# Kernel tuning notes

Measured on AMD Instinct MI355X. Metric: run time of the kernel, lower is better.

## Reference

```python
import jax, jax.numpy as jnp
import numpy as np

D = 512   # in_dim
W = 8     # window
B = 8192  # batch


def _l2norm(x):
    # matches torch.nn.functional.normalize(p=2, dim=-1, eps=1e-12)
    n = jnp.linalg.norm(x, axis=-1, keepdims=True)
    return x / jnp.maximum(n, 1e-12)


def setup_inputs() -> dict:
    key = jax.random.key(0)
    ks = jax.random.split(key, 15)
    s = 1.0 / np.sqrt(D)  # torch nn.Linear default init range
    u = lambda k, shape: jax.random.uniform(k, shape, jnp.float32, -s, s)
    return {
        "x": jax.random.normal(ks[0], (B, (2 * W + 1) * D), jnp.float32),
        "Wq": u(ks[1], (D, D)), "bq": u(ks[2], (D,)),
        "Wkc": u(ks[3], (D, D)), "bkc": u(ks[4], (D,)),
        "Wkp": u(ks[5], (W, D, D)), "bkp": u(ks[6], (W, D)),
        "Wkn": u(ks[7], (W, D, D)), "bkn": u(ks[8], (W, D)),
        "Wfp": u(ks[9], (W, D, D)), "bfp": u(ks[10], (W, D)),
        "Wfn": u(ks[11], (W, D, D)), "bfn": u(ks[12], (W, D)),
        "Wfc": u(ks[13], (D, D)), "bfc": u(ks[14], (D,)),
    }


def reference(x, Wq, bq, Wkc, bkc, Wkp, bkp, Wkn, bkn, Wfp, bfp, Wfn, bfn, Wfc, bfc):
    b = x.shape[0]
    xp = x[:, : W * D].reshape(b, W, D)             # prev chunks [B,W,D]
    xc = x[:, W * D : (W + 1) * D]                  # center      [B,D]
    xn = x[:, (W + 1) * D :].reshape(b, W, D)       # next chunks [B,W,D]

    q = xc @ Wq.T + bq                              # [B,D]
    kc = xc @ Wkc.T + bkc
    attn_c = jnp.sum(q * kc, axis=-1, keepdims=True)  # [B,1]

    # per-offset key projections, batched over the W offsets
    kp = jnp.einsum('bwd,wed->bwe', xp, Wkp) + bkp  # [B,W,D]
    kn = jnp.einsum('bwd,wed->bwe', xn, Wkn) + bkn
    ap = jnp.einsum('bd,bwd->bw', q, kp)            # [B,W]
    an = jnp.einsum('bd,bwd->bw', q, kn)

    xc_ = (xc * attn_c
           + jnp.einsum('bw,bwd->bd', ap, xp)
           + jnp.einsum('bw,bwd->bd', an, xn))

    # per-offset feed-forward + l2 normalize (dropout = identity at eval)
    xp_out = _l2norm(jnp.einsum('bwd,wed->bwe', xp, Wfp) + bfp)
    xn_out = _l2norm(jnp.einsum('bwd,wed->bwe', xn, Wfn) + bfn)

    xc_ = _l2norm(xc_)
    xc_ = xc_ @ Wfc.T + bfc
    xc_ = _l2norm(xc_ + xc)

    return jnp.concatenate([xp_out.reshape(b, W * D), xc_, xn_out.reshape(b, W * D)], axis=1)
```

## Files before the change

kernel.cpp:

```cpp
#include <hip/hip_runtime.h>
#include <stdint.h>

#define D 512
#define NW 8
#define BATCH 8192
#define XROW 8704
#define BM 128
#define BK 64
#define MAT 262144

typedef __attribute__((ext_vector_type(8))) short bf16x8;
typedef __attribute__((ext_vector_type(4))) float f32x4;

struct Params {
  const float* x;
  const float* bq; const float* bkc;
  const float* bkp; const float* bkn;
  const float* bfp; const float* bfn;
  const float* bfc;
  const unsigned short* Wb;
  unsigned short* qw;
  unsigned short* kcw;
  float* ap; float* an;
  float* xcn;
  float* out;
};

__device__ __forceinline__ unsigned short f2bf(float f) {
  union { float f; unsigned u; } v; v.f = f;
  unsigned u = v.u + 0x7FFFu + ((v.u >> 16) & 1u);
  return (unsigned short)(u >> 16);
}
__device__ __forceinline__ float bf2f(unsigned short h) {
  union { unsigned u; float f; } v; v.u = ((unsigned)h) << 16;
  return v.f;
}

__global__ void convert_weights(const float* Wq, const float* Wkc, const float* Wkp,
                                const float* Wkn, const float* Wfp, const float* Wfn,
                                const float* Wfc, unsigned short* outw) {
  const int total4 = 35 * MAT / 4;
  for (int i4 = blockIdx.x * blockDim.x + threadIdx.x; i4 < total4;
       i4 += gridDim.x * blockDim.x) {
    int idx = i4 * 4;
    int m = idx >> 18;
    int e = idx & (MAT - 1);
    const float* src;
    if (m == 0)       src = Wq + e;
    else if (m == 1)  src = Wkc + e;
    else if (m < 10)  src = Wkp + (size_t)(m - 2) * MAT + e;
    else if (m < 18)  src = Wkn + (size_t)(m - 10) * MAT + e;
    else if (m < 26)  src = Wfp + (size_t)(m - 18) * MAT + e;
    else if (m < 34)  src = Wfn + (size_t)(m - 26) * MAT + e;
    else              src = Wfc + e;
    float4 v = *reinterpret_cast<const float4*>(src);
    ushort4 o;
    o.x = f2bf(v.x); o.y = f2bf(v.y); o.z = f2bf(v.z); o.w = f2bf(v.w);
    *reinterpret_cast<ushort4*>(outw + idx) = o;
  }
}

__launch_bounds__(512)
__global__ void gemm_mega(Params p, int launch_id) {
  __shared__ unsigned short Alds[BM * BK];
  __shared__ unsigned short Blds[D * BK];

  const int nchunk = gridDim.x >> 3;
  const int swz  = (blockIdx.x & 7) * nchunk + (blockIdx.x >> 3);
  const int unit = swz >> 6;
  const int mb   = swz & 63;
  const int t    = threadIdx.x;
  const int lane = t & 63;
  const int wave = t >> 6;
  const int wm   = wave >> 2;
  const int wn   = wave & 3;

  const float* Aptr = p.x;
  int lda = XROW;
  int aofs = 0;
  const unsigned short* Wm = p.Wb;
  const float* bias = p.bq;
  int epi = 0;
  int outofs = 0;
  float* dotdst = nullptr;
  int wofs = 0;

  if (launch_id == 0) {
    if (unit == 0)      { aofs = 8 * D; Wm = p.Wb;            bias = p.bq;  epi = 0; }
    else if (unit == 1) { aofs = 8 * D; Wm = p.Wb + MAT;      bias = p.bkc; epi = 1; }
    else if (unit < 10) { int w = unit - 2;  aofs = w * D;
                          Wm = p.Wb + (size_t)(18 + w) * MAT; bias = p.bfp + w * D;
                          epi = 2; outofs = w * D; }
    else                { int w = unit - 10; aofs = (9 + w) * D;
                          Wm = p.Wb + (size_t)(26 + w) * MAT; bias = p.bfn + w * D;
                          epi = 2; outofs = (9 + w) * D; }
  } else if (launch_id == 1) {
    if (unit < 8) { int w = unit;     aofs = w * D;
                    Wm = p.Wb + (size_t)(2 + w) * MAT;  bias = p.bkp + w * D;
                    epi = 3; dotdst = p.ap; wofs = w; }
    else          { int w = unit - 8; aofs = (9 + w) * D;
                    Wm = p.Wb + (size_t)(10 + w) * MAT; bias = p.bkn + w * D;
                    epi = 3; dotdst = p.an; wofs = w; }
  } else {
    Aptr = p.xcn; lda = D; aofs = 0;
    Wm = p.Wb + (size_t)34 * MAT; bias = p.bfc; epi = 4; outofs = 8 * D;
  }

  const int row0 = mb * BM;

  f32x4 acc[4][8];
#pragma unroll
  for (int m = 0; m < 4; ++m)
#pragma unroll
    for (int n = 0; n < 8; ++n)
      acc[m][n] = (f32x4){0.f, 0.f, 0.f, 0.f};

  const int ar = t >> 2;
  const int ak = (t & 3) * 16;
  const float* a_src = Aptr + (size_t)(row0 + ar) * lda + aofs + ak;

  char* albase = (char*)Alds;
  char* blbase = (char*)Blds;

  for (int kt = 0; kt < 8; ++kt) {
    const int k0 = kt * BK;
    float4 av0 = *reinterpret_cast<const float4*>(a_src + k0);
    float4 av1 = *reinterpret_cast<const float4*>(a_src + k0 + 4);
    float4 av2 = *reinterpret_cast<const float4*>(a_src + k0 + 8);
    float4 av3 = *reinterpret_cast<const float4*>(a_src + k0 + 12);
    {
      bf16x8 pk;
      pk[0] = (short)f2bf(av0.x); pk[1] = (short)f2bf(av0.y);
      pk[2] = (short)f2bf(av0.z); pk[3] = (short)f2bf(av0.w);
      pk[4] = (short)f2bf(av1.x); pk[5] = (short)f2bf(av1.y);
      pk[6] = (short)f2bf(av1.z); pk[7] = (short)f2bf(av1.w);
      int bo = (ar << 7) + (ak << 1);
      *reinterpret_cast<bf16x8*>(albase + (bo ^ ((bo >> 3) & 0x70))) = pk;
      pk[0] = (short)f2bf(av2.x); pk[1] = (short)f2bf(av2.y);
      pk[2] = (short)f2bf(av2.z); pk[3] = (short)f2bf(av2.w);
      pk[4] = (short)f2bf(av3.x); pk[5] = (short)f2bf(av3.y);
      pk[6] = (short)f2bf(av3.z); pk[7] = (short)f2bf(av3.w);
      bo += 16;
      *reinterpret_cast<bf16x8*>(albase + (bo ^ ((bo >> 3) & 0x70))) = pk;
    }
#pragma unroll
    for (int i = 0; i < 8; ++i) {
      int o = i * 8192 + wave * 1024 + lane * 16;
      int Ls = o ^ ((o >> 3) & 0x70);
      const unsigned short* src = Wm + (size_t)(Ls >> 7) * D + k0 + ((Ls & 127) >> 1);
      __builtin_amdgcn_global_load_lds(
          (const __attribute__((address_space(1))) unsigned*)src,
          (__attribute__((address_space(3))) unsigned*)(blbase + i * 8192 + wave * 1024),
          16, 0, 0);
    }
    __syncthreads();
#pragma unroll
    for (int ks = 0; ks < 2; ++ks) {
      const int kb = ks * 64 + ((lane >> 4) << 4);
      bf16x8 af[4], bfr[8];
#pragma unroll
      for (int m = 0; m < 4; ++m) {
        int r = wm * 64 + m * 16 + (lane & 15);
        int bo = (r << 7) + kb;
        af[m] = *reinterpret_cast<const bf16x8*>(albase + (bo ^ ((bo >> 3) & 0x70)));
      }
#pragma unroll
      for (int n = 0; n < 8; ++n) {
        int r = wn * 128 + n * 16 + (lane & 15);
        int bo = (r << 7) + kb;
        bfr[n] = *reinterpret_cast<const bf16x8*>(blbase + (bo ^ ((bo >> 3) & 0x70)));
      }
#pragma unroll
      for (int m = 0; m < 4; ++m)
#pragma unroll
        for (int n = 0; n < 8; ++n)
          acc[m][n] = __builtin_amdgcn_mfma_f32_16x16x32_bf16(af[m], bfr[n], acc[m][n], 0, 0, 0);
    }
    __syncthreads();
  }

  float* red = (float*)Alds;
  const int rj = (lane >> 4) * 4;
  const int cl = lane & 15;
  float bv[8];
#pragma unroll
  for (int n = 0; n < 8; ++n) bv[n] = bias[wn * 128 + n * 16 + cl];
#pragma unroll
  for (int m = 0; m < 4; ++m)
#pragma unroll
    for (int n = 0; n < 8; ++n)
#pragma unroll
      for (int j = 0; j < 4; ++j)
        acc[m][n][j] += bv[n];

  if (epi <= 1) {
    unsigned short* dst = (epi == 0) ? p.qw : p.kcw;
#pragma unroll
    for (int m = 0; m < 4; ++m)
#pragma unroll
      for (int j = 0; j < 4; ++j) {
        int r = wm * 64 + m * 16 + rj + j;
#pragma unroll
        for (int n = 0; n < 8; ++n) {
          int col = wn * 128 + n * 16 + cl;
          dst[(size_t)(row0 + r) * D + col] = f2bf(acc[m][n][j]);
        }
      }
  } else if (epi == 3) {
    if (t < BM) red[t] = 0.f;
    __syncthreads();
#pragma unroll
    for (int m = 0; m < 4; ++m)
#pragma unroll
      for (int j = 0; j < 4; ++j) {
        int r = wm * 64 + m * 16 + rj + j;
        float s = 0.f;
#pragma unroll
        for (int n = 0; n < 8; ++n) {
          int col = wn * 128 + n * 16 + cl;
          s += acc[m][n][j] * bf2f(p.qw[(size_t)(row0 + r) * D + col]);
        }
        s += __shfl_xor(s, 1); s += __shfl_xor(s, 2);
        s += __shfl_xor(s, 4); s += __shfl_xor(s, 8);
        if (cl == 0) atomicAdd(&red[r], s);
      }
    __syncthreads();
    if (t < BM) dotdst[(size_t)(row0 + t) * NW + wofs] = red[t];
  } else {
    if (epi == 4) {
#pragma unroll
      for (int m = 0; m < 4; ++m)
#pragma unroll
        for (int j = 0; j < 4; ++j) {
          int r = wm * 64 + m * 16 + rj + j;
#pragma unroll
          for (int n = 0; n < 8; ++n) {
            int col = wn * 128 + n * 16 + cl;
            acc[m][n][j] += p.x[(size_t)(row0 + r) * XROW + 8 * D + col];
          }
        }
    }
    if (t < BM) red[t] = 0.f;
    __syncthreads();
#pragma unroll
    for (int m = 0; m < 4; ++m)
#pragma unroll
      for (int j = 0; j < 4; ++j) {
        int r = wm * 64 + m * 16 + rj + j;
        float s = 0.f;
#pragma unroll
        for (int n = 0; n < 8; ++n) s += acc[m][n][j] * acc[m][n][j];
        s += __shfl_xor(s, 1); s += __shfl_xor(s, 2);
        s += __shfl_xor(s, 4); s += __shfl_xor(s, 8);
        if (cl == 0) atomicAdd(&red[r], s);
      }
    __syncthreads();
#pragma unroll
    for (int m = 0; m < 4; ++m)
#pragma unroll
      for (int j = 0; j < 4; ++j) {
        int r = wm * 64 + m * 16 + rj + j;
        float sc = 1.f / fmaxf(sqrtf(red[r]), 1e-12f);
#pragma unroll
        for (int n = 0; n < 8; ++n) {
          int col = wn * 128 + n * 16 + cl;
          p.out[(size_t)(row0 + r) * XROW + outofs + col] = acc[m][n][j] * sc;
        }
      }
  }
}

__launch_bounds__(128)
__global__ void combine(Params p) {
  __shared__ float sbuf[2];
  __shared__ float swt[16];
  const int b = blockIdx.x;
  const int t = threadIdx.x;
  const float* xrow = p.x + (size_t)b * XROW;

  const ushort4 q4 = reinterpret_cast<const ushort4*>(p.qw + (size_t)b * D)[t];
  const ushort4 c4 = reinterpret_cast<const ushort4*>(p.kcw + (size_t)b * D)[t];
  float s = bf2f(q4.x) * bf2f(c4.x) + bf2f(q4.y) * bf2f(c4.y) +
            bf2f(q4.z) * bf2f(c4.z) + bf2f(q4.w) * bf2f(c4.w);
  for (int m = 32; m >= 1; m >>= 1) s += __shfl_xor(s, m);
  if ((t & 63) == 0) sbuf[t >> 6] = s;
  if (t < 8)       swt[t] = p.ap[(size_t)b * NW + t];
  else if (t < 16) swt[t] = p.an[(size_t)b * NW + (t - 8)];
  __syncthreads();
  const float att = sbuf[0] + sbuf[1];

  float4 xc4 = reinterpret_cast<const float4*>(xrow + 8 * D)[t];
  float4 v;
  v.x = xc4.x * att; v.y = xc4.y * att; v.z = xc4.z * att; v.w = xc4.w * att;
#pragma unroll
  for (int w = 0; w < 8; ++w) {
    float aw = swt[w], nw2 = swt[8 + w];
    float4 xp4 = reinterpret_cast<const float4*>(xrow + w * D)[t];
    float4 xn4 = reinterpret_cast<const float4*>(xrow + (9 + w) * D)[t];
    v.x += aw * xp4.x + nw2 * xn4.x;
    v.y += aw * xp4.y + nw2 * xn4.y;
    v.z += aw * xp4.z + nw2 * xn4.z;
    v.w += aw * xp4.w + nw2 * xn4.w;
  }
  float ss = v.x * v.x + v.y * v.y + v.z * v.z + v.w * v.w;
  __syncthreads();
  for (int m = 32; m >= 1; m >>= 1) ss += __shfl_xor(ss, m);
  if ((t & 63) == 0) sbuf[t >> 6] = ss;
  __syncthreads();
  float sc = 1.f / fmaxf(sqrtf(sbuf[0] + sbuf[1]), 1e-12f);
  float4 o; o.x = v.x * sc; o.y = v.y * sc; o.z = v.z * sc; o.w = v.w * sc;
  reinterpret_cast<float4*>(p.xcn + (size_t)b * D)[t] = o;
}

extern "C" void kernel_launch(void* const* d_in, const int* in_sizes, int n_in,
                              void* d_out, int out_size, void* d_ws, size_t ws_size,
                              hipStream_t stream) {
  const float* x   = (const float*)d_in[0];
  const float* Wq  = (const float*)d_in[1];
  const float* bq  = (const float*)d_in[2];
  const float* Wkc = (const float*)d_in[3];
  const float* bkc = (const float*)d_in[4];
  const float* Wkp = (const float*)d_in[5];
  const float* bkp = (const float*)d_in[6];
  const float* Wkn = (const float*)d_in[7];
  const float* bkn = (const float*)d_in[8];
  const float* Wfp = (const float*)d_in[9];
  const float* bfp = (const float*)d_in[10];
  const float* Wfn = (const float*)d_in[11];
  const float* bfn = (const float*)d_in[12];
  const float* Wfc = (const float*)d_in[13];
  const float* bfc = (const float*)d_in[14];

  char* ws = (char*)d_ws;
  unsigned short* Wb  = (unsigned short*)ws;
  unsigned short* qw  = (unsigned short*)(ws + 18350080);
  unsigned short* kcw = (unsigned short*)(ws + 26738688);
  float* ap  = (float*)(ws + 35127296);
  float* an  = (float*)(ws + 35389440);
  float* xcn = (float*)(ws + 35651584);

  Params p { x, bq, bkc, bkp, bkn, bfp, bfn, bfc, Wb, qw, kcw, ap, an, xcn, (float*)d_out };

  hipLaunchKernelGGL(convert_weights, dim3(2048), dim3(256), 0, stream,
                     Wq, Wkc, Wkp, Wkn, Wfp, Wfn, Wfc, Wb);
  hipLaunchKernelGGL(gemm_mega, dim3(18 * 64), dim3(512), 0, stream, p, 0);
  hipLaunchKernelGGL(gemm_mega, dim3(16 * 64), dim3(512), 0, stream, p, 1);
  hipLaunchKernelGGL(combine,   dim3(8192),   dim3(128), 0, stream, p);
  hipLaunchKernelGGL(gemm_mega, dim3(64),     dim3(512), 0, stream, p, 2);
}
```

Baseline: 870.4 us.

## Pre-convert x to bf16 and double-buffer GEMM loads with async global-to-LDS

Adds a bf16 copy of the whole input x to the conversion kernel, so the GEMM can load A tiles with direct global-to-LDS loads, the same way it loads weights. The GEMM main loop becomes a two-stage double-buffered pipeline with BK=32 and 16 k-steps, using explicit vmcnt waits, barriers and raised priority around the MFMA block. The combine kernel now writes its normalized output as bf16 for the final GEMM. The aim is to overlap memory traffic with compute and drop in-loop fp32 conversion, at the cost of an extra full pass over x (read fp32, write bf16) and a larger workspace.

```diff
diff --git a/kernel.cpp b/kernel.cpp
--- a/kernel.cpp
+++ b/kernel.cpp
@@ -6,7 +6,8 @@
 #define BATCH 8192
 #define XROW 8704
 #define BM 128
-#define BK 64
+#define BK 32
+#define KT 16
 #define MAT 262144
 
 typedef __attribute__((ext_vector_type(8))) short bf16x8;
@@ -19,10 +20,11 @@
   const float* bfp; const float* bfn;
   const float* bfc;
   const unsigned short* Wb;
+  const unsigned short* xb;
   unsigned short* qw;
   unsigned short* kcw;
   float* ap; float* an;
-  float* xcn;
+  unsigned short* xcn;
   float* out;
 };
 
@@ -36,34 +38,47 @@
   return v.f;
 }
 
-__global__ void convert_weights(const float* Wq, const float* Wkc, const float* Wkp,
-                                const float* Wkn, const float* Wfp, const float* Wfn,
-                                const float* Wfc, unsigned short* outw) {
-  const int total4 = 35 * MAT / 4;
+__global__ void convert_all(const float* x, const float* Wq, const float* Wkc,
+                            const float* Wkp, const float* Wkn, const float* Wfp,
+                            const float* Wfn, const float* Wfc,
+                            unsigned short* Wb, unsigned short* xb) {
+  const int totW = 35 * MAT;
+  const int total4 = (totW + BATCH * XROW) / 4;
   for (int i4 = blockIdx.x * blockDim.x + threadIdx.x; i4 < total4;
        i4 += gridDim.x * blockDim.x) {
     int idx = i4 * 4;
-    int m = idx >> 18;
-    int e = idx & (MAT - 1);
     const float* src;
-    if (m == 0)       src = Wq + e;
-    else if (m == 1)  src = Wkc + e;
-    else if (m < 10)  src = Wkp + (size_t)(m - 2) * MAT + e;
-    else if (m < 18)  src = Wkn + (size_t)(m - 10) * MAT + e;
-    else if (m < 26)  src = Wfp + (size_t)(m - 18) * MAT + e;
-    else if (m < 34)  src = Wfn + (size_t)(m - 26) * MAT + e;
-    else              src = Wfc + e;
+    unsigned short* dst;
+    if (idx < totW) {
+      int m = idx >> 18;
+      int e = idx & (MAT - 1);
+      if (m == 0)       src = Wq + e;
+      else if (m == 1)  src = Wkc + e;
+      else if (m < 10)  src = Wkp + (size_t)(m - 2) * MAT + e;
+      else if (m < 18)  src = Wkn + (size_t)(m - 10) * MAT + e;
+      else if (m < 26)  src = Wfp + (size_t)(m - 18) * MAT + e;
+      else if (m < 34)  src = Wfn + (size_t)(m - 26) * MAT + e;
+      else              src = Wfc + e;
+      dst = Wb + idx;
+    } else {
+      int e = idx - totW;
+      src = x + e;
+      dst = xb + e;
+    }
     float4 v = *reinterpret_cast<const float4*>(src);
     ushort4 o;
     o.x = f2bf(v.x); o.y = f2bf(v.y); o.z = f2bf(v.z); o.w = f2bf(v.w);
-    *reinterpret_cast<ushort4*>(outw + idx) = o;
-  }
-}
+    *reinterpret_cast<ushort4*>(dst) = o;
+  }
+}
+
+#define GLOAD(SRC, DST) __builtin_amdgcn_global_load_lds( \
+    (const __attribute__((address_space(1))) unsigned*)(SRC), \
+    (__attribute__((address_space(3))) unsigned*)(DST), 16, 0, 0)
 
 __launch_bounds__(512)
 __global__ void gemm_mega(Params p, int launch_id) {
-  __shared__ unsigned short Alds[BM * BK];
-  __shared__ unsigned short Blds[D * BK];
+  __shared__ unsigned short lds2[2][20480];
 
   const int nchunk = gridDim.x >> 3;
   const int swz  = (blockIdx.x & 7) * nchunk + (blockIdx.x >> 3);
@@ -75,7 +90,7 @@
   const int wm   = wave >> 2;
   const int wn   = wave & 3;
 
-  const float* Aptr = p.x;
+  const unsigned short* Aab = p.xb;
   int lda = XROW;
   int aofs = 0;
   const unsigned short* Wm = p.Wb;
@@ -102,7 +117,7 @@
                     Wm = p.Wb + (size_t)(10 + w) * MAT; bias = p.bkn + w * D;
                     epi = 3; dotdst = p.an; wofs = w; }
   } else {
-    Aptr = p.xcn; lda = D; aofs = 0;
+    Aab = p.xcn; lda = D; aofs = 0;
     Wm = p.Wb + (size_t)34 * MAT; bias = p.bfc; epi = 4; outofs = 8 * D;
   }
 
@@ -115,71 +130,66 @@
     for (int n = 0; n < 8; ++n)
       acc[m][n] = (f32x4){0.f, 0.f, 0.f, 0.f};
 
-  const int ar = t >> 2;
-  const int ak = (t & 3) * 16;
-  const float* a_src = Aptr + (size_t)(row0 + ar) * lda + aofs + ak;
-
-  char* albase = (char*)Alds;
-  char* blbase = (char*)Blds;
-
-  for (int kt = 0; kt < 8; ++kt) {
-    const int k0 = kt * BK;
-    float4 av0 = *reinterpret_cast<const float4*>(a_src + k0);
-    float4 av1 = *reinterpret_cast<const float4*>(a_src + k0 + 4);
-    float4 av2 = *reinterpret_cast<const float4*>(a_src + k0 + 8);
-    float4 av3 = *reinterpret_cast<const float4*>(a_src + k0 + 12);
-    {
-      bf16x8 pk;
-      pk[0] = (short)f2bf(av0.x); pk[1] = (short)f2bf(av0.y);
-      pk[2] = (short)f2bf(av0.z); pk[3] = (short)f2bf(av0.w);
-      pk[4] = (short)f2bf(av1.x); pk[5] = (short)f2bf(av1.y);
-      pk[6] = (short)f2bf(av1.z); pk[7] = (short)f2bf(av1.w);
-      int bo = (ar << 7) + (ak << 1);
-      *reinterpret_cast<bf16x8*>(albase + (bo ^ ((bo >> 3) & 0x70))) = pk;
-      pk[0] = (short)f2bf(av2.x); pk[1] = (short)f2bf(av2.y);
-      pk[2] = (short)f2bf(av2.z); pk[3] = (short)f2bf(av2.w);
-      pk[4] = (short)f2bf(av3.x); pk[5] = (short)f2bf(av3.y);
-      pk[6] = (short)f2bf(av3.z); pk[7] = (short)f2bf(av3.w);
-      bo += 16;
-      *reinterpret_cast<bf16x8*>(albase + (bo ^ ((bo >> 3) & 0x70))) = pk;
-    }
-#pragma unroll
-    for (int i = 0; i < 8; ++i) {
-      int o = i * 8192 + wave * 1024 + lane * 16;
-      int Ls = o ^ ((o >> 3) & 0x70);
-      const unsigned short* src = Wm + (size_t)(Ls >> 7) * D + k0 + ((Ls & 127) >> 1);
-      __builtin_amdgcn_global_load_lds(
-          (const __attribute__((address_space(1))) unsigned*)src,
-          (__attribute__((address_space(3))) unsigned*)(blbase + i * 8192 + wave * 1024),
-          16, 0, 0);
-    }
-    __syncthreads();
-#pragma unroll
-    for (int ks = 0; ks < 2; ++ks) {
-      const int kb = ks * 64 + ((lane >> 4) << 4);
-      bf16x8 af[4], bfr[8];
-#pragma unroll
-      for (int m = 0; m < 4; ++m) {
-        int r = wm * 64 + m * 16 + (lane & 15);
-        int bo = (r << 7) + kb;
-        af[m] = *reinterpret_cast<const bf16x8*>(albase + (bo ^ ((bo >> 3) & 0x70)));
-      }
-#pragma unroll
-      for (int n = 0; n < 8; ++n) {
-        int r = wn * 128 + n * 16 + (lane & 15);
-        int bo = (r << 7) + kb;
-        bfr[n] = *reinterpret_cast<const bf16x8*>(blbase + (bo ^ ((bo >> 3) & 0x70)));
-      }
-#pragma unroll
-      for (int m = 0; m < 4; ++m)
-#pragma unroll
-        for (int n = 0; n < 8; ++n)
-          acc[m][n] = __builtin_amdgcn_mfma_f32_16x16x32_bf16(af[m], bfr[n], acc[m][n], 0, 0, 0);
-    }
-    __syncthreads();
-  }
-
-  float* red = (float*)Alds;
+  const unsigned short* aST;
+  {
+    int o = t * 16; int Ls = o ^ ((o >> 3) & 0x70);
+    aST = Aab + (size_t)(row0 + (Ls >> 6)) * lda + aofs + ((Ls & 63) >> 1);
+  }
+  const unsigned short* bSTa[4];
+#pragma unroll
+  for (int j = 0; j < 4; ++j) {
+    int o = t * 16 + j * 8192; int Ls = o ^ ((o >> 3) & 0x70);
+    bSTa[j] = Wm + (size_t)(Ls >> 6) * D + ((Ls & 63) >> 1);
+  }
+
+#define STAGE(S, KE) do { \
+    GLOAD(aST + (KE), &lds2[S][0] + wave * 512); \
+    _Pragma("unroll") \
+    for (int j = 0; j < 4; ++j) \
+      GLOAD(bSTa[j] + (KE), &lds2[S][4096 + j * 4096] + wave * 512); \
+  } while (0)
+
+#define CSTEP(S) do { \
+    bf16x8 af[4], bfr[8]; \
+    const int kb = (lane >> 4) * 16; \
+    _Pragma("unroll") for (int m = 0; m < 4; ++m) { \
+      int L = ((wm * 64 + m * 16 + (lane & 15)) << 6) + kb; \
+      af[m] = *reinterpret_cast<const bf16x8*>((const char*)&lds2[S][0] + (L ^ ((L >> 3) & 0x70))); } \
+    _Pragma("unroll") for (int n = 0; n < 8; ++n) { \
+      int L = ((wn * 128 + n * 16 + (lane & 15)) << 6) + kb; \
+      bfr[n] = *reinterpret_cast<const bf16x8*>((const char*)&lds2[S][4096] + (L ^ ((L >> 3) & 0x70))); } \
+    asm volatile("s_waitcnt lgkmcnt(0)" ::: "memory"); \
+    __builtin_amdgcn_sched_barrier(0); \
+    __builtin_amdgcn_s_setprio(1); \
+    _Pragma("unroll") for (int m = 0; m < 4; ++m) \
+      _Pragma("unroll") for (int n = 0; n < 8; ++n) \
+        acc[m][n] = __builtin_amdgcn_mfma_f32_16x16x32_bf16(af[m], bfr[n], acc[m][n], 0, 0, 0); \
+    __builtin_amdgcn_s_setprio(0); \
+  } while (0)
+
+  STAGE(0, 0);
+  for (int kt = 0; kt < KT - 1; ++kt) {
+    const int cur = kt & 1;
+    STAGE(cur ^ 1, (kt + 1) * 32);
+    __builtin_amdgcn_sched_barrier(0);
+    asm volatile("s_waitcnt vmcnt(5)" ::: "memory");
+    __builtin_amdgcn_sched_barrier(0);
+    __builtin_amdgcn_s_barrier();
+    __builtin_amdgcn_sched_barrier(0);
+    CSTEP(cur);
+    __builtin_amdgcn_sched_barrier(0);
+    __builtin_amdgcn_s_barrier();
+  }
+  __builtin_amdgcn_sched_barrier(0);
+  asm volatile("s_waitcnt vmcnt(0)" ::: "memory");
+  __builtin_amdgcn_sched_barrier(0);
+  __builtin_amdgcn_s_barrier();
+  __builtin_amdgcn_sched_barrier(0);
+  CSTEP(1);
+  __builtin_amdgcn_sched_barrier(0);
+  __builtin_amdgcn_s_barrier();
+
+  float* red = (float*)(&lds2[0][0]);
   const int rj = (lane >> 4) * 4;
   const int cl = lane & 15;
   float bv[8];
@@ -268,6 +278,8 @@
         }
       }
   }
+#undef STAGE
+#undef CSTEP
 }
 
 __launch_bounds__(128)
@@ -308,8 +320,10 @@
   if ((t & 63) == 0) sbuf[t >> 6] = ss;
   __syncthreads();
   float sc = 1.f / fmaxf(sqrtf(sbuf[0] + sbuf[1]), 1e-12f);
-  float4 o; o.x = v.x * sc; o.y = v.y * sc; o.z = v.z * sc; o.w = v.w * sc;
-  reinterpret_cast<float4*>(p.xcn + (size_t)b * D)[t] = o;
+  ushort4 o;
+  o.x = f2bf(v.x * sc); o.y = f2bf(v.y * sc);
+  o.z = f2bf(v.z * sc); o.w = f2bf(v.w * sc);
+  reinterpret_cast<ushort4*>(p.xcn + (size_t)b * D)[t] = o;
 }
 
 extern "C" void kernel_launch(void* const* d_in, const int* in_sizes, int n_in,
@@ -333,16 +347,17 @@
 
   char* ws = (char*)d_ws;
   unsigned short* Wb  = (unsigned short*)ws;
-  unsigned short* qw  = (unsigned short*)(ws + 18350080);
-  unsigned short* kcw = (unsigned short*)(ws + 26738688);
-  float* ap  = (float*)(ws + 35127296);
-  float* an  = (float*)(ws + 35389440);
-  float* xcn = (float*)(ws + 35651584);
-
-  Params p { x, bq, bkc, bkp, bkn, bfp, bfn, bfc, Wb, qw, kcw, ap, an, xcn, (float*)d_out };
-
-  hipLaunchKernelGGL(convert_weights, dim3(2048), dim3(256), 0, stream,
-                     Wq, Wkc, Wkp, Wkn, Wfp, Wfn, Wfc, Wb);
+  unsigned short* xb  = (unsigned short*)(ws + 18350080);
+  unsigned short* qw  = (unsigned short*)(ws + 160956416);
+  unsigned short* kcw = (unsigned short*)(ws + 169345024);
+  float* ap  = (float*)(ws + 177733632);
+  float* an  = (float*)(ws + 177995776);
+  unsigned short* xcn = (unsigned short*)(ws + 178257920);
+
+  Params p { x, bq, bkc, bkp, bkn, bfp, bfn, bfc, Wb, xb, qw, kcw, ap, an, xcn, (float*)d_out };
+
+  hipLaunchKernelGGL(convert_all, dim3(4096), dim3(256), 0, stream,
+                     x, Wq, Wkc, Wkp, Wkn, Wfp, Wfn, Wfc, Wb, xb);
   hipLaunchKernelGGL(gemm_mega, dim3(18 * 64), dim3(512), 0, stream, p, 0);
   hipLaunchKernelGGL(gemm_mega, dim3(16 * 64), dim3(512), 0, stream, p, 1);
   hipLaunchKernelGGL(combine,   dim3(8192),   dim3(128), 0, stream, p);
```

New measurement: 946.0 us. +8.7%, slower.

## Double-buffer LDS tiles with BK=32 and prefetch next K-step during MFMA

Applied to the files above, without the earlier changes.

Restructures the GEMM main loop into a two-stage LDS ping-pong with a smaller K tile. The next tile's weights are loaded asynchronously into LDS and the next activations are converted while the current tile runs through MFMA, with one barrier per step instead of two. It also precomputes the LDS offsets, uses explicit waitcnt and sched barriers, and raises priority around the MFMA block. The aim is to hide global load latency behind compute. The cost is twice as many K iterations and hand-tuned vmcnt counts, which are fragile if the compiler reorders memory operations.

```diff
diff --git a/kernel.cpp b/kernel.cpp
--- a/kernel.cpp
+++ b/kernel.cpp
@@ -6,8 +6,10 @@
 #define BATCH 8192
 #define XROW 8704
 #define BM 128
-#define BK 64
+#define BK 32
+#define KT 16
 #define MAT 262144
+#define BUFB 40960
 
 typedef __attribute__((ext_vector_type(8))) short bf16x8;
 typedef __attribute__((ext_vector_type(4))) float f32x4;
@@ -60,10 +62,13 @@
   }
 }
 
+#define GLOAD(SRC, DST) __builtin_amdgcn_global_load_lds( \
+    (const __attribute__((address_space(1))) unsigned*)(SRC), \
+    (__attribute__((address_space(3))) unsigned*)(DST), 16, 0, 0)
+
 __launch_bounds__(512)
 __global__ void gemm_mega(Params p, int launch_id) {
-  __shared__ unsigned short Alds[BM * BK];
-  __shared__ unsigned short Blds[D * BK];
+  __shared__ unsigned short lds2[2][BUFB / 2];
 
   const int nchunk = gridDim.x >> 3;
   const int swz  = (blockIdx.x & 7) * nchunk + (blockIdx.x >> 3);
@@ -115,71 +120,96 @@
     for (int n = 0; n < 8; ++n)
       acc[m][n] = (f32x4){0.f, 0.f, 0.f, 0.f};
 
-  const int ar = t >> 2;
-  const int ak = (t & 3) * 16;
-  const float* a_src = Aptr + (size_t)(row0 + ar) * lda + aofs + ak;
-
-  char* albase = (char*)Alds;
-  char* blbase = (char*)Blds;
-
-  for (int kt = 0; kt < 8; ++kt) {
-    const int k0 = kt * BK;
-    float4 av0 = *reinterpret_cast<const float4*>(a_src + k0);
-    float4 av1 = *reinterpret_cast<const float4*>(a_src + k0 + 4);
-    float4 av2 = *reinterpret_cast<const float4*>(a_src + k0 + 8);
-    float4 av3 = *reinterpret_cast<const float4*>(a_src + k0 + 12);
-    {
-      bf16x8 pk;
-      pk[0] = (short)f2bf(av0.x); pk[1] = (short)f2bf(av0.y);
-      pk[2] = (short)f2bf(av0.z); pk[3] = (short)f2bf(av0.w);
-      pk[4] = (short)f2bf(av1.x); pk[5] = (short)f2bf(av1.y);
-      pk[6] = (short)f2bf(av1.z); pk[7] = (short)f2bf(av1.w);
-      int bo = (ar << 7) + (ak << 1);
-      *reinterpret_cast<bf16x8*>(albase + (bo ^ ((bo >> 3) & 0x70))) = pk;
-      pk[0] = (short)f2bf(av2.x); pk[1] = (short)f2bf(av2.y);
-      pk[2] = (short)f2bf(av2.z); pk[3] = (short)f2bf(av2.w);
-      pk[4] = (short)f2bf(av3.x); pk[5] = (short)f2bf(av3.y);
-      pk[6] = (short)f2bf(av3.z); pk[7] = (short)f2bf(av3.w);
-      bo += 16;
-      *reinterpret_cast<bf16x8*>(albase + (bo ^ ((bo >> 3) & 0x70))) = pk;
+  char* lbase = (char*)lds2;
+
+  const int ar  = t >> 2;
+  const int akb = (t & 3) * 16;
+  const float* a_src = Aptr + (size_t)(row0 + ar) * lda + aofs + (t & 3) * 8;
+
+  const unsigned short* bSTa[4];
+#pragma unroll
+  for (int j = 0; j < 4; ++j) {
+    int o = j * 8192 + t * 16;
+    int Ls = o ^ ((o >> 3) & 0x70);
+    bSTa[j] = Wm + (size_t)(Ls >> 6) * D + ((Ls & 63) >> 1);
+  }
+
+  const int kb = (lane >> 4) * 16;
+  int aoff[4], boff[8];
+#pragma unroll
+  for (int m = 0; m < 4; ++m) {
+    int L = ((wm * 64 + m * 16 + (lane & 15)) << 6) + kb;
+    aoff[m] = L ^ ((L >> 3) & 0x70);
+  }
+#pragma unroll
+  for (int n = 0; n < 8; ++n) {
+    int L = ((wn * 128 + n * 16 + (lane & 15)) << 6) + kb;
+    boff[n] = 8192 + (L ^ ((L >> 3) & 0x70));
+  }
+
+#define STAGE_B(S, KE) do { \
+    _Pragma("unroll") \
+    for (int j = 0; j < 4; ++j) \
+      GLOAD(bSTa[j] + (KE), lbase + (S) * BUFB + 8192 + j * 8192 + t * 16); \
+  } while (0)
+
+#define CVTWR(S, A0, A1) do { \
+    bf16x8 pk; \
+    pk[0] = (short)f2bf((A0).x); pk[1] = (short)f2bf((A0).y); \
+    pk[2] = (short)f2bf((A0).z); pk[3] = (short)f2bf((A0).w); \
+    pk[4] = (short)f2bf((A1).x); pk[5] = (short)f2bf((A1).y); \
+    pk[6] = (short)f2bf((A1).z); pk[7] = (short)f2bf((A1).w); \
+    int bo = (ar << 6) + akb; \
+    *reinterpret_cast<bf16x8*>(lbase + (S) * BUFB + (bo ^ ((bo >> 3) & 0x70))) = pk; \
+  } while (0)
+
+#define CSTEP(S) do { \
+    bf16x8 af[4], bfr[8]; \
+    _Pragma("unroll") for (int m = 0; m < 4; ++m) \
+      af[m] = *reinterpret_cast<const bf16x8*>(lbase + (S) * BUFB + aoff[m]); \
+    _Pragma("unroll") for (int n = 0; n < 8; ++n) \
+      bfr[n] = *reinterpret_cast<const bf16x8*>(lbase + (S) * BUFB + boff[n]); \
+    asm volatile("s_waitcnt lgkmcnt(0)" ::: "memory"); \
+    __builtin_amdgcn_sched_barrier(0); \
+    __builtin_amdgcn_s_setprio(1); \
+    _Pragma("unroll") for (int m = 0; m < 4; ++m) \
+      _Pragma("unroll") for (int n = 0; n < 8; ++n) \
+        acc[m][n] = __builtin_amdgcn_mfma_f32_16x16x32_bf16(af[m], bfr[n], acc[m][n], 0, 0, 0); \
+    __builtin_amdgcn_s_setprio(0); \
+  } while (0)
+
+  float4 a0 = *reinterpret_cast<const float4*>(a_src);
+  float4 a1 = *reinterpret_cast<const float4*>(a_src + 4);
+  STAGE_B(0, 0);
+  CVTWR(0, a0, a1);
+  a0 = *reinterpret_cast<const float4*>(a_src + BK);
+  a1 = *reinterpret_cast<const float4*>(a_src + BK + 4);
+  asm volatile("s_waitcnt vmcnt(2)" ::: "memory");
+  asm volatile("s_waitcnt lgkmcnt(0)" ::: "memory");
+  __builtin_amdgcn_sched_barrier(0);
+  __builtin_amdgcn_s_barrier();
+
+#pragma unroll 2
+  for (int kt = 0; kt < KT; ++kt) {
+    const int cur = kt & 1;
+    if (kt < KT - 1) {
+      STAGE_B(cur ^ 1, (kt + 1) * BK);
+      CVTWR(cur ^ 1, a0, a1);
+      if (kt < KT - 2) {
+        a0 = *reinterpret_cast<const float4*>(a_src + (kt + 2) * BK);
+        a1 = *reinterpret_cast<const float4*>(a_src + (kt + 2) * BK + 4);
+      }
     }
-#pragma unroll
-    for (int i = 0; i < 8; ++i) {
-      int o = i * 8192 + wave * 1024 + lane * 16;
-      int Ls = o ^ ((o >> 3) & 0x70);
-      const unsigned short* src = Wm + (size_t)(Ls >> 7) * D + k0 + ((Ls & 127) >> 1);
-      __builtin_amdgcn_global_load_lds(
-          (const __attribute__((address_space(1))) unsigned*)src,
-          (__attribute__((address_space(3))) unsigned*)(blbase + i * 8192 + wave * 1024),
-          16, 0, 0);
-    }
-    __syncthreads();
-#pragma unroll
-    for (int ks = 0; ks < 2; ++ks) {
-      const int kb = ks * 64 + ((lane >> 4) << 4);
-      bf16x8 af[4], bfr[8];
-#pragma unroll
-      for (int m = 0; m < 4; ++m) {
-        int r = wm * 64 + m * 16 + (lane & 15);
-        int bo = (r << 7) + kb;
-        af[m] = *reinterpret_cast<const bf16x8*>(albase + (bo ^ ((bo >> 3) & 0x70)));
-      }
-#pragma unroll
-      for (int n = 0; n < 8; ++n) {
-        int r = wn * 128 + n * 16 + (lane & 15);
-        int bo = (r << 7) + kb;
-        bfr[n] = *reinterpret_cast<const bf16x8*>(blbase + (bo ^ ((bo >> 3) & 0x70)));
-      }
-#pragma unroll
-      for (int m = 0; m < 4; ++m)
-#pragma unroll
-        for (int n = 0; n < 8; ++n)
-          acc[m][n] = __builtin_amdgcn_mfma_f32_16x16x32_bf16(af[m], bfr[n], acc[m][n], 0, 0, 0);
-    }
-    __syncthreads();
-  }
-
-  float* red = (float*)Alds;
+    CSTEP(cur);
+    if (kt < KT - 2)
+      asm volatile("s_waitcnt vmcnt(2)" ::: "memory");
+    else if (kt == KT - 2)
+      asm volatile("s_waitcnt vmcnt(0)" ::: "memory");
+    __builtin_amdgcn_sched_barrier(0);
+    __builtin_amdgcn_s_barrier();
+  }
+
+  float* red = (float*)lbase;
   const int rj = (lane >> 4) * 4;
   const int cl = lane & 15;
   float bv[8];
@@ -268,6 +298,9 @@
         }
       }
   }
+#undef STAGE_B
+#undef CVTWR
+#undef CSTEP
 }
 
 __launch_bounds__(128)
```

After: 831.7 us. 4.5% less time.
